# Kernel optimization log

Measured on AMD Instinct MI355X. Metric: run time of the kernel, lower is better.

The kernel has to match this reference:

```python
import jax, jax.numpy as jnp
import numpy as np

B = 32768
F = 256
H1 = 16
H2 = 8

def setup_inputs() -> dict:
    key = jax.random.key(0)
    ks = jax.random.split(key, 9)
    x = jax.random.normal(ks[0], (B, F), dtype=jnp.float32)
    # Stacked per-feature MLP params (one UnivariateNetwork per feature)
    W1 = jax.random.normal(ks[1], (F, H1), dtype=jnp.float32) * (1.0 / np.sqrt(1))
    b1 = jax.random.normal(ks[2], (F, H1), dtype=jnp.float32) * 0.05
    W2 = jax.random.normal(ks[3], (F, H1, H2), dtype=jnp.float32) * (1.0 / np.sqrt(H1))
    b2 = jax.random.normal(ks[4], (F, H2), dtype=jnp.float32) * 0.05
    W3 = jax.random.normal(ks[5], (F, H2), dtype=jnp.float32) * (1.0 / np.sqrt(H2))
    b3 = jax.random.normal(ks[6], (F,), dtype=jnp.float32) * 0.05
    theta = jax.random.uniform(ks[7], (F,), dtype=jnp.float32) * 0.05
    bias = jnp.zeros((1,), dtype=jnp.float32)
    return {"x": x, "W1": W1, "b1": b1, "W2": W2, "b2": b2,
            "W3": W3, "b3": b3, "theta": theta, "bias": bias}

def reference(x, W1, b1, W2, b2, W3, b3, theta, bias):
    # Batched per-feature MLP: 1 -> H1 -> H2 -> 1 with ELU, all features at once.
    h1 = jax.nn.elu(x[:, :, None] * W1[None, :, :] + b1[None, :, :])      # [B, F, H1]
    h2 = jax.nn.elu(jnp.einsum('bfh,fhk->bfk', h1, W2) + b2[None, :, :])  # [B, F, H2]
    Z = jnp.einsum('bfk,fk->bf', h2, W3) + b3[None, :]                    # [B, F]
    weights = jax.nn.softplus(theta)                                      # [F]
    y_pred = Z @ weights + bias                                           # [B]
    return (y_pred, weights, Z)
```

## Files before the change

### kernel.cpp

```cpp
#include <hip/hip_runtime.h>

#define NB 32768
#define NF 256
#define H1 16
#define HH 8
#define H2 8
#define R_PER_BLOCK 64
#define CHUNK 16
#define NT 512

__device__ __forceinline__ float elu_f(float v) {
    return v > 0.0f ? v : (__expf(v) - 1.0f);
}

__global__ __launch_bounds__(NT, 4)
void nul_kernel(const float* __restrict__ x,
                const float* __restrict__ W1, const float* __restrict__ b1,
                const float* __restrict__ W2, const float* __restrict__ b2,
                const float* __restrict__ W3, const float* __restrict__ b3,
                const float* __restrict__ theta, const float* __restrict__ bias,
                float* __restrict__ y_out, float* __restrict__ w_out,
                float* __restrict__ z_out) {
    const int tid  = threadIdx.x;
    const int f    = tid >> 1;
    const int half = tid & 1;
    const int rowBase = blockIdx.x * R_PER_BLOCK;

    float w1v[HH], b1v[HH];
    {
        const float4* p = reinterpret_cast<const float4*>(W1 + f * H1 + half * HH);
        float4 v0 = p[0], v1 = p[1];
        w1v[0]=v0.x; w1v[1]=v0.y; w1v[2]=v0.z; w1v[3]=v0.w;
        w1v[4]=v1.x; w1v[5]=v1.y; w1v[6]=v1.z; w1v[7]=v1.w;
    }
    {
        const float4* p = reinterpret_cast<const float4*>(b1 + f * H1 + half * HH);
        float4 v0 = p[0], v1 = p[1];
        b1v[0]=v0.x; b1v[1]=v0.y; b1v[2]=v0.z; b1v[3]=v0.w;
        b1v[4]=v1.x; b1v[5]=v1.y; b1v[6]=v1.z; b1v[7]=v1.w;
    }
    float w2v[HH * H2];
    {
        const float4* p = reinterpret_cast<const float4*>(W2 + f * H1 * H2 + half * HH * H2);
        #pragma unroll
        for (int i = 0; i < (HH * H2) / 4; ++i) {
            float4 v = p[i];
            w2v[4*i]=v.x; w2v[4*i+1]=v.y; w2v[4*i+2]=v.z; w2v[4*i+3]=v.w;
        }
    }
    float b2i[H2];
    {
        const float4* p = reinterpret_cast<const float4*>(b2 + f * H2);
        float4 v0 = p[0], v1 = p[1];
        const float m = (half == 0) ? 1.0f : 0.0f;
        b2i[0]=v0.x*m; b2i[1]=v0.y*m; b2i[2]=v0.z*m; b2i[3]=v0.w*m;
        b2i[4]=v1.x*m; b2i[5]=v1.y*m; b2i[6]=v1.z*m; b2i[7]=v1.w*m;
    }
    float w3v[H2];
    {
        const float4* p = reinterpret_cast<const float4*>(W3 + f * H2);
        float4 v0 = p[0], v1 = p[1];
        w3v[0]=v0.x; w3v[1]=v0.y; w3v[2]=v0.z; w3v[3]=v0.w;
        w3v[4]=v1.x; w3v[5]=v1.y; w3v[6]=v1.z; w3v[7]=v1.w;
    }
    const float b3v   = b3[f];
    const float th    = theta[f];
    const float wv    = logf(1.0f + __expf(th));
    const float biasv = bias[0];

    if (blockIdx.x == 0 && half == 0) w_out[f] = wv;

    __shared__ float P[CHUNK][NF + 1];

    float xnext = x[rowBase * NF + f];

    for (int c = 0; c < R_PER_BLOCK; c += CHUNK) {
        #pragma unroll 1
        for (int r = 0; r < CHUNK; ++r) {
            const int row = rowBase + c + r;
            const float xv = xnext;
            int nrow = row + 1; if (nrow >= NB) nrow = row;
            xnext = x[nrow * NF + f];

            float acc[H2];
            #pragma unroll
            for (int k = 0; k < H2; ++k) acc[k] = b2i[k];
            #pragma unroll
            for (int h = 0; h < HH; ++h) {
                const float h1 = elu_f(fmaf(xv, w1v[h], b1v[h]));
                #pragma unroll
                for (int k = 0; k < H2; ++k)
                    acc[k] = fmaf(h1, w2v[h * H2 + k], acc[k]);
            }

            #pragma unroll
            for (int k = 0; k < H2; ++k)
                acc[k] += __shfl_xor(acc[k], 1, 64);

            float z = b3v;
            #pragma unroll
            for (int k = 0; k < H2; ++k)
                z = fmaf(elu_f(acc[k]), w3v[k], z);

            if (half == 0) {
                z_out[row * NF + f] = z;
                P[r][f] = wv * z;
            }
        }
        __syncthreads();
        if (tid < 256) {
            const int rr = tid >> 4;
            const int l  = tid & 15;
            float s = 0.0f;
            #pragma unroll
            for (int i = 0; i < 16; ++i) s += P[rr][i * 16 + l];
            #pragma unroll
            for (int o = 8; o > 0; o >>= 1) s += __shfl_down(s, o, 16);
            if (l == 0) y_out[rowBase + c + rr] = s + biasv;
        }
        __syncthreads();
    }
}

extern "C" void kernel_launch(void* const* d_in, const int* in_sizes, int n_in,
                              void* d_out, int out_size, void* d_ws, size_t ws_size,
                              hipStream_t stream) {
    const float* x     = (const float*)d_in[0];
    const float* W1    = (const float*)d_in[1];
    const float* b1    = (const float*)d_in[2];
    const float* W2    = (const float*)d_in[3];
    const float* b2    = (const float*)d_in[4];
    const float* W3    = (const float*)d_in[5];
    const float* b3    = (const float*)d_in[6];
    const float* theta = (const float*)d_in[7];
    const float* bias  = (const float*)d_in[8];

    float* y_out = (float*)d_out;
    float* w_out = y_out + NB;
    float* z_out = w_out + NF;

    nul_kernel<<<NB / R_PER_BLOCK, NT, 0, stream>>>(
        x, W1, b1, W2, b2, W3, b3, theta, bias, y_out, w_out, z_out);
}
```

Baseline: 172.9 us.

## Use one thread per feature and process two rows per iteration

Each thread now owns a whole feature's MLP (all 16 hidden units) instead of splitting the hidden units across two lanes. This removes the cross-lane shuffle reduction and the idle half-lane stores. Rows are processed in pairs so the weight registers are reused across two independent FMA chains, which adds instruction-level parallelism. The cost is a much larger register footprint (128+ weights per thread), which is why the block is halved to 256 threads with a lower occupancy target.

```diff
diff --git a/kernel.cpp b/kernel.cpp
--- a/kernel.cpp
+++ b/kernel.cpp
@@ -3,17 +3,16 @@
 #define NB 32768
 #define NF 256
 #define H1 16
-#define HH 8
 #define H2 8
 #define R_PER_BLOCK 64
 #define CHUNK 16
-#define NT 512
+#define NT 256
 
 __device__ __forceinline__ float elu_f(float v) {
     return v > 0.0f ? v : (__expf(v) - 1.0f);
 }
 
-__global__ __launch_bounds__(NT, 4)
+__global__ __launch_bounds__(NT, 2)
 void nul_kernel(const float* __restrict__ x,
                 const float* __restrict__ W1, const float* __restrict__ b1,
                 const float* __restrict__ W2, const float* __restrict__ b2,
@@ -21,96 +20,107 @@
                 const float* __restrict__ theta, const float* __restrict__ bias,
                 float* __restrict__ y_out, float* __restrict__ w_out,
                 float* __restrict__ z_out) {
-    const int tid  = threadIdx.x;
-    const int f    = tid >> 1;
-    const int half = tid & 1;
+    const int f = threadIdx.x;
     const int rowBase = blockIdx.x * R_PER_BLOCK;
 
-    float w1v[HH], b1v[HH];
+    float w1v[H1], b1v[H1], w2v[H1 * H2], b2v[H2], w3v[H2];
     {
-        const float4* p = reinterpret_cast<const float4*>(W1 + f * H1 + half * HH);
-        float4 v0 = p[0], v1 = p[1];
-        w1v[0]=v0.x; w1v[1]=v0.y; w1v[2]=v0.z; w1v[3]=v0.w;
-        w1v[4]=v1.x; w1v[5]=v1.y; w1v[6]=v1.z; w1v[7]=v1.w;
+        const float4* p = reinterpret_cast<const float4*>(W1 + f * H1);
+        #pragma unroll
+        for (int i = 0; i < H1 / 4; ++i) {
+            float4 v = p[i];
+            w1v[4*i] = v.x; w1v[4*i+1] = v.y; w1v[4*i+2] = v.z; w1v[4*i+3] = v.w;
+        }
     }
     {
-        const float4* p = reinterpret_cast<const float4*>(b1 + f * H1 + half * HH);
-        float4 v0 = p[0], v1 = p[1];
-        b1v[0]=v0.x; b1v[1]=v0.y; b1v[2]=v0.z; b1v[3]=v0.w;
-        b1v[4]=v1.x; b1v[5]=v1.y; b1v[6]=v1.z; b1v[7]=v1.w;
-    }
-    float w2v[HH * H2];
-    {
-        const float4* p = reinterpret_cast<const float4*>(W2 + f * H1 * H2 + half * HH * H2);
+        const float4* p = reinterpret_cast<const float4*>(b1 + f * H1);
         #pragma unroll
-        for (int i = 0; i < (HH * H2) / 4; ++i) {
+        for (int i = 0; i < H1 / 4; ++i) {
             float4 v = p[i];
-            w2v[4*i]=v.x; w2v[4*i+1]=v.y; w2v[4*i+2]=v.z; w2v[4*i+3]=v.w;
+            b1v[4*i] = v.x; b1v[4*i+1] = v.y; b1v[4*i+2] = v.z; b1v[4*i+3] = v.w;
         }
     }
-    float b2i[H2];
+    {
+        const float4* p = reinterpret_cast<const float4*>(W2 + f * H1 * H2);
+        #pragma unroll
+        for (int i = 0; i < (H1 * H2) / 4; ++i) {
+            float4 v = p[i];
+            w2v[4*i] = v.x; w2v[4*i+1] = v.y; w2v[4*i+2] = v.z; w2v[4*i+3] = v.w;
+        }
+    }
     {
         const float4* p = reinterpret_cast<const float4*>(b2 + f * H2);
-        float4 v0 = p[0], v1 = p[1];
-        const float m = (half == 0) ? 1.0f : 0.0f;
-        b2i[0]=v0.x*m; b2i[1]=v0.y*m; b2i[2]=v0.z*m; b2i[3]=v0.w*m;
-        b2i[4]=v1.x*m; b2i[5]=v1.y*m; b2i[6]=v1.z*m; b2i[7]=v1.w*m;
+        #pragma unroll
+        for (int i = 0; i < H2 / 4; ++i) {
+            float4 v = p[i];
+            b2v[4*i] = v.x; b2v[4*i+1] = v.y; b2v[4*i+2] = v.z; b2v[4*i+3] = v.w;
+        }
     }
-    float w3v[H2];
     {
         const float4* p = reinterpret_cast<const float4*>(W3 + f * H2);
-        float4 v0 = p[0], v1 = p[1];
-        w3v[0]=v0.x; w3v[1]=v0.y; w3v[2]=v0.z; w3v[3]=v0.w;
-        w3v[4]=v1.x; w3v[5]=v1.y; w3v[6]=v1.z; w3v[7]=v1.w;
+        #pragma unroll
+        for (int i = 0; i < H2 / 4; ++i) {
+            float4 v = p[i];
+            w3v[4*i] = v.x; w3v[4*i+1] = v.y; w3v[4*i+2] = v.z; w3v[4*i+3] = v.w;
+        }
     }
     const float b3v   = b3[f];
     const float th    = theta[f];
     const float wv    = logf(1.0f + __expf(th));
     const float biasv = bias[0];
 
-    if (blockIdx.x == 0 && half == 0) w_out[f] = wv;
+    if (blockIdx.x == 0) w_out[f] = wv;
 
     __shared__ float P[CHUNK][NF + 1];
 
-    float xnext = x[rowBase * NF + f];
+    const float* xp = x + rowBase * NF + f;
+
+    float xa = xp[0];
+    float xb = xp[NF];
 
     for (int c = 0; c < R_PER_BLOCK; c += CHUNK) {
         #pragma unroll 1
-        for (int r = 0; r < CHUNK; ++r) {
-            const int row = rowBase + c + r;
-            const float xv = xnext;
-            int nrow = row + 1; if (nrow >= NB) nrow = row;
-            xnext = x[nrow * NF + f];
+        for (int r = 0; r < CHUNK; r += 2) {
+            const int row0 = rowBase + c + r;
 
-            float acc[H2];
+            int p0 = c + r + 2; if (p0 > R_PER_BLOCK - 1) p0 = R_PER_BLOCK - 1;
+            int p1 = c + r + 3; if (p1 > R_PER_BLOCK - 1) p1 = R_PER_BLOCK - 1;
+            const float xa2 = xp[p0 * NF];
+            const float xb2 = xp[p1 * NF];
+
+            float acc0[H2], acc1[H2];
             #pragma unroll
-            for (int k = 0; k < H2; ++k) acc[k] = b2i[k];
+            for (int k = 0; k < H2; ++k) { acc0[k] = b2v[k]; acc1[k] = b2v[k]; }
             #pragma unroll
-            for (int h = 0; h < HH; ++h) {
-                const float h1 = elu_f(fmaf(xv, w1v[h], b1v[h]));
+            for (int h = 0; h < H1; ++h) {
+                const float ha = elu_f(fmaf(xa, w1v[h], b1v[h]));
+                const float hb = elu_f(fmaf(xb, w1v[h], b1v[h]));
                 #pragma unroll
-                for (int k = 0; k < H2; ++k)
-                    acc[k] = fmaf(h1, w2v[h * H2 + k], acc[k]);
+                for (int k = 0; k < H2; ++k) {
+                    const float w = w2v[h * H2 + k];
+                    acc0[k] = fmaf(ha, w, acc0[k]);
+                    acc1[k] = fmaf(hb, w, acc1[k]);
+                }
             }
 
+            float z0 = b3v, z1 = b3v;
             #pragma unroll
-            for (int k = 0; k < H2; ++k)
-                acc[k] += __shfl_xor(acc[k], 1, 64);
+            for (int k = 0; k < H2; ++k) {
+                z0 = fmaf(elu_f(acc0[k]), w3v[k], z0);
+                z1 = fmaf(elu_f(acc1[k]), w3v[k], z1);
+            }
 
-            float z = b3v;
-            #pragma unroll
-            for (int k = 0; k < H2; ++k)
-                z = fmaf(elu_f(acc[k]), w3v[k], z);
+            z_out[row0 * NF + f]       = z0;
+            z_out[(row0 + 1) * NF + f] = z1;
+            P[r][f]     = wv * z0;
+            P[r + 1][f] = wv * z1;
 
-            if (half == 0) {
-                z_out[row * NF + f] = z;
-                P[r][f] = wv * z;
-            }
+            xa = xa2; xb = xb2;
         }
         __syncthreads();
-        if (tid < 256) {
-            const int rr = tid >> 4;
-            const int l  = tid & 15;
+        {
+            const int rr = threadIdx.x >> 4;
+            const int l  = threadIdx.x & 15;
             float s = 0.0f;
             #pragma unroll
             for (int i = 0; i < 16; ++i) s += P[rr][i * 16 + l];
```

Result: slower. 653.0 us (+277.6%).

## Split into per-feature wave Z kernel and separate row-reduction Y kernel

Applied to the files above, without the earlier changes.

Maps each wave to one feature, with lanes covering 64 rows. The per-feature weights are then wave-uniform, so half of W2 and b1 are moved into scalar registers via readfirstlane. This removes the two-thread-per-feature split, the shuffle exchange and the duplicated first-layer work. The weighted row sum for y moves into a second kernel that reads Z back with coalesced float4 loads. The trade-off is strided, uncoalesced x loads and z stores (one row per lane), plus an extra launch and a re-read of Z.

```diff
diff --git a/kernel.cpp b/kernel.cpp
--- a/kernel.cpp
+++ b/kernel.cpp
@@ -3,122 +3,139 @@
 #define NB 32768
 #define NF 256
 #define H1 16
-#define HH 8
 #define H2 8
-#define R_PER_BLOCK 64
-#define CHUNK 16
-#define NT 512
+#define ROWS_PER_BLOCK 1024
+#define ITERS (ROWS_PER_BLOCK / 64)
+#define FPB 4
+#define NT (FPB * 64)
 
 __device__ __forceinline__ float elu_f(float v) {
     return v > 0.0f ? v : (__expf(v) - 1.0f);
 }
+__device__ __forceinline__ float rfl(float v) {
+    return __int_as_float(__builtin_amdgcn_readfirstlane(__float_as_int(v)));
+}
 
 __global__ __launch_bounds__(NT, 4)
-void nul_kernel(const float* __restrict__ x,
-                const float* __restrict__ W1, const float* __restrict__ b1,
-                const float* __restrict__ W2, const float* __restrict__ b2,
-                const float* __restrict__ W3, const float* __restrict__ b3,
-                const float* __restrict__ theta, const float* __restrict__ bias,
-                float* __restrict__ y_out, float* __restrict__ w_out,
-                float* __restrict__ z_out) {
-    const int tid  = threadIdx.x;
-    const int f    = tid >> 1;
-    const int half = tid & 1;
-    const int rowBase = blockIdx.x * R_PER_BLOCK;
+void z_kernel(const float* __restrict__ x,  const float* __restrict__ W1,
+              const float* __restrict__ b1, const float* __restrict__ W2,
+              const float* __restrict__ b2, const float* __restrict__ W3,
+              const float* __restrict__ b3, float* __restrict__ z_out) {
+    const int wave = threadIdx.x >> 6;
+    const int lane = threadIdx.x & 63;
+    const int f    = blockIdx.y * FPB + wave;
+    const int rowBase = blockIdx.x * ROWS_PER_BLOCK;
 
-    float w1v[HH], b1v[HH];
+    float s_w2[8 * H2];
+    float w2h[8 * H2];
     {
-        const float4* p = reinterpret_cast<const float4*>(W1 + f * H1 + half * HH);
-        float4 v0 = p[0], v1 = p[1];
-        w1v[0]=v0.x; w1v[1]=v0.y; w1v[2]=v0.z; w1v[3]=v0.w;
-        w1v[4]=v1.x; w1v[5]=v1.y; w1v[6]=v1.z; w1v[7]=v1.w;
-    }
-    {
-        const float4* p = reinterpret_cast<const float4*>(b1 + f * H1 + half * HH);
-        float4 v0 = p[0], v1 = p[1];
-        b1v[0]=v0.x; b1v[1]=v0.y; b1v[2]=v0.z; b1v[3]=v0.w;
-        b1v[4]=v1.x; b1v[5]=v1.y; b1v[6]=v1.z; b1v[7]=v1.w;
-    }
-    float w2v[HH * H2];
-    {
-        const float4* p = reinterpret_cast<const float4*>(W2 + f * H1 * H2 + half * HH * H2);
+        const float4* p = reinterpret_cast<const float4*>(W2 + f * H1 * H2);
         #pragma unroll
-        for (int i = 0; i < (HH * H2) / 4; ++i) {
+        for (int i = 0; i < 16; ++i) {
             float4 v = p[i];
-            w2v[4*i]=v.x; w2v[4*i+1]=v.y; w2v[4*i+2]=v.z; w2v[4*i+3]=v.w;
+            s_w2[4*i]   = rfl(v.x); s_w2[4*i+1] = rfl(v.y);
+            s_w2[4*i+2] = rfl(v.z); s_w2[4*i+3] = rfl(v.w);
+        }
+        #pragma unroll
+        for (int i = 0; i < 16; ++i) {
+            float4 v = p[16 + i];
+            w2h[4*i] = v.x; w2h[4*i+1] = v.y; w2h[4*i+2] = v.z; w2h[4*i+3] = v.w;
         }
     }
-    float b2i[H2];
+    float w1v[H1], s_b1[H1];
+    {
+        const float4* pw = reinterpret_cast<const float4*>(W1 + f * H1);
+        const float4* pb = reinterpret_cast<const float4*>(b1 + f * H1);
+        #pragma unroll
+        for (int i = 0; i < 4; ++i) {
+            float4 v = pw[i];
+            w1v[4*i] = v.x; w1v[4*i+1] = v.y; w1v[4*i+2] = v.z; w1v[4*i+3] = v.w;
+        }
+        #pragma unroll
+        for (int i = 0; i < 4; ++i) {
+            float4 v = pb[i];
+            s_b1[4*i]   = rfl(v.x); s_b1[4*i+1] = rfl(v.y);
+            s_b1[4*i+2] = rfl(v.z); s_b1[4*i+3] = rfl(v.w);
+        }
+    }
+    float b2v[H2], w3v[H2];
     {
         const float4* p = reinterpret_cast<const float4*>(b2 + f * H2);
         float4 v0 = p[0], v1 = p[1];
-        const float m = (half == 0) ? 1.0f : 0.0f;
-        b2i[0]=v0.x*m; b2i[1]=v0.y*m; b2i[2]=v0.z*m; b2i[3]=v0.w*m;
-        b2i[4]=v1.x*m; b2i[5]=v1.y*m; b2i[6]=v1.z*m; b2i[7]=v1.w*m;
+        b2v[0]=v0.x; b2v[1]=v0.y; b2v[2]=v0.z; b2v[3]=v0.w;
+        b2v[4]=v1.x; b2v[5]=v1.y; b2v[6]=v1.z; b2v[7]=v1.w;
     }
-    float w3v[H2];
     {
         const float4* p = reinterpret_cast<const float4*>(W3 + f * H2);
         float4 v0 = p[0], v1 = p[1];
         w3v[0]=v0.x; w3v[1]=v0.y; w3v[2]=v0.z; w3v[3]=v0.w;
         w3v[4]=v1.x; w3v[5]=v1.y; w3v[6]=v1.z; w3v[7]=v1.w;
     }
-    const float b3v   = b3[f];
-    const float th    = theta[f];
-    const float wv    = logf(1.0f + __expf(th));
-    const float biasv = bias[0];
+    const float b3v = b3[f];
 
-    if (blockIdx.x == 0 && half == 0) w_out[f] = wv;
+    int off = (rowBase + lane) * NF + f;
+    float xv = x[off];
 
-    __shared__ float P[CHUNK][NF + 1];
+    #pragma unroll 1
+    for (int it = 0; it < ITERS; ++it) {
+        const int noff = off + 64 * NF;
+        const float xn = x[(it + 1 < ITERS) ? noff : off];
 
-    float xnext = x[rowBase * NF + f];
+        float acc[H2];
+        #pragma unroll
+        for (int k = 0; k < H2; ++k) acc[k] = b2v[k];
 
-    for (int c = 0; c < R_PER_BLOCK; c += CHUNK) {
-        #pragma unroll 1
-        for (int r = 0; r < CHUNK; ++r) {
-            const int row = rowBase + c + r;
-            const float xv = xnext;
-            int nrow = row + 1; if (nrow >= NB) nrow = row;
-            xnext = x[nrow * NF + f];
-
-            float acc[H2];
-            #pragma unroll
-            for (int k = 0; k < H2; ++k) acc[k] = b2i[k];
-            #pragma unroll
-            for (int h = 0; h < HH; ++h) {
-                const float h1 = elu_f(fmaf(xv, w1v[h], b1v[h]));
-                #pragma unroll
-                for (int k = 0; k < H2; ++k)
-                    acc[k] = fmaf(h1, w2v[h * H2 + k], acc[k]);
-            }
-
+        #pragma unroll
+        for (int h = 0; h < 8; ++h) {
+            const float h1 = elu_f(fmaf(xv, w1v[h], s_b1[h]));
             #pragma unroll
             for (int k = 0; k < H2; ++k)
-                acc[k] += __shfl_xor(acc[k], 1, 64);
-
-            float z = b3v;
+                acc[k] = fmaf(h1, s_w2[h * H2 + k], acc[k]);
+        }
+        #pragma unroll
+        for (int h = 0; h < 8; ++h) {
+            const float h1 = elu_f(fmaf(xv, w1v[8 + h], s_b1[8 + h]));
             #pragma unroll
             for (int k = 0; k < H2; ++k)
-                z = fmaf(elu_f(acc[k]), w3v[k], z);
+                acc[k] = fmaf(h1, w2h[h * H2 + k], acc[k]);
+        }
 
-            if (half == 0) {
-                z_out[row * NF + f] = z;
-                P[r][f] = wv * z;
-            }
-        }
-        __syncthreads();
-        if (tid < 256) {
-            const int rr = tid >> 4;
-            const int l  = tid & 15;
-            float s = 0.0f;
-            #pragma unroll
-            for (int i = 0; i < 16; ++i) s += P[rr][i * 16 + l];
-            #pragma unroll
-            for (int o = 8; o > 0; o >>= 1) s += __shfl_down(s, o, 16);
-            if (l == 0) y_out[rowBase + c + rr] = s + biasv;
-        }
-        __syncthreads();
+        float z = b3v;
+        #pragma unroll
+        for (int k = 0; k < H2; ++k)
+            z = fmaf(elu_f(acc[k]), w3v[k], z);
+
+        z_out[off] = z;
+        off = noff; xv = xn;
+    }
+}
+
+#define NT2 256
+#define ROWS2 64
+__global__ __launch_bounds__(NT2, 4)
+void y_kernel(const float* __restrict__ z, const float* __restrict__ theta,
+              const float* __restrict__ bias, float* __restrict__ y_out,
+              float* __restrict__ w_out) {
+    __shared__ __align__(16) float wls[NF];
+    const int tid = threadIdx.x;
+    {
+        const float th = theta[tid];
+        const float w  = logf(1.0f + __expf(th));
+        wls[tid] = w;
+        if (blockIdx.x == 0) w_out[tid] = w;
+    }
+    __syncthreads();
+    const int wave = tid >> 6, lane = tid & 63;
+    const float4 w4 = reinterpret_cast<const float4*>(wls)[lane];
+    const float biasv = bias[0];
+    #pragma unroll 1
+    for (int r = 0; r < ROWS2 / 4; ++r) {
+        const int row = blockIdx.x * ROWS2 + wave * (ROWS2 / 4) + r;
+        const float4 zv = reinterpret_cast<const float4*>(z + row * NF)[lane];
+        float s = zv.x * w4.x + zv.y * w4.y + zv.z * w4.z + zv.w * w4.w;
+        #pragma unroll
+        for (int o = 32; o > 0; o >>= 1) s += __shfl_down(s, o, 64);
+        if (lane == 0) y_out[row] = s + biasv;
     }
 }
 
@@ -139,6 +156,7 @@
     float* w_out = y_out + NB;
     float* z_out = w_out + NF;
 
-    nul_kernel<<<NB / R_PER_BLOCK, NT, 0, stream>>>(
-        x, W1, b1, W2, b2, W3, b3, theta, bias, y_out, w_out, z_out);
+    dim3 grid1(NB / ROWS_PER_BLOCK, NF / FPB);
+    z_kernel<<<grid1, NT, 0, stream>>>(x, W1, b1, W2, b2, W3, b3, z_out);
+    y_kernel<<<NB / ROWS2, NT2, 0, stream>>>(z_out, theta, bias, y_out, w_out);
 }
```

Result: faster. 162.4 us (-6.1%).
